# Kernel optimization log

Hardware: AMD Instinct MI355X
Metric: run time of the kernel (lower is better)

## Reference

```python
import jax, jax.numpy as jnp
import numpy as np

MAX_NUM_CENTERS = 100
CENTER_IGNORE_PX = 3
SIGMA = 2.0   # center_gt_blur
KSIZE = 21    # GaussianLayer kernel size (ReflectionPad2d(10) + Conv2d(k=21))


def _gauss_kernel():
    r = KSIZE // 2
    x = jnp.arange(-r, r + 1, dtype=jnp.float32)
    g = jnp.exp(-0.5 * (x / SIGMA) ** 2)
    g = g / g.sum()
    return jnp.outer(g, g)  # [21,21], sums to 1 (matches scipy gaussian_filter of a delta)


def _gaussian_blur(x):
    # x: [B,H,W] -> depthwise 21x21 gaussian with reflect padding (GaussianLayer)
    r = KSIZE // 2
    k = _gauss_kernel()[None, None]  # [1,1,21,21]
    xp = jnp.pad(x[:, None], ((0, 0), (0, 0), (r, r), (r, r)), mode="reflect")
    y = jax.lax.conv_general_dilated(xp, k, (1, 1), "VALID",
                                     dimension_numbers=("NCHW", "OIHW", "NCHW"))
    return y[:, 0]


def setup_inputs() -> dict:
    key = jax.random.key(0)
    k1, k2 = jax.random.split(key)
    B, H, W = 8, 768, 768
    instances = jax.random.randint(k1, (B, 1, H, W), 0, MAX_NUM_CENTERS, dtype=jnp.int32)
    centers = jax.random.uniform(k2, (B, MAX_NUM_CENTERS, 2), dtype=jnp.float32) * (H - 1) + 1.0
    return {"instances": instances, "centers": centers}


def reference(instances, centers):
    B, _, H, W = instances.shape
    inst = instances[:, 0]                                # [B,H,W]
    col = jnp.arange(W, dtype=jnp.float32)                # xym_s[0][i,j] = j
    row = jnp.arange(H, dtype=jnp.float32)[:, None]       # xym_s[1][i,j] = i

    valid = inst > 0                                      # instance_mask
    has_inst = jnp.any(valid, axis=(1, 2)).astype(jnp.float32)  # len(unique)>1 gate

    # per-pixel nearest-center gather: center = centers[b, id-1]
    idx = jnp.clip(inst - 1, 0, MAX_NUM_CENTERS - 1)
    c = centers[jnp.arange(B)[:, None, None], idx]        # [B,H,W,2]
    gt_cx = jnp.where(valid, c[..., 1], -10000.0)         # gt_center_x (swapped coords)
    gt_cy = jnp.where(valid, c[..., 0], -10000.0)

    gt_X = gt_cx - row                                    # gt_center_x - xym_s[1]
    gt_Y = gt_cy - col                                    # gt_center_y - xym_s[0]

    near = (jnp.abs(gt_X) < CENTER_IGNORE_PX) & (jnp.abs(gt_Y) < CENTER_IGNORE_PX)
    # batches with no instances skip the block -> ignore stays all-ones
    ignore = jnp.where(has_inst[:, None, None] > 0, (~near).astype(jnp.float32), 1.0)

    m = valid.astype(jnp.float32)
    R = jnp.sqrt(gt_X ** 2 + gt_Y ** 2) * m
    theta_raw = jnp.arctan2(gt_Y, gt_X)
    theta = theta_raw * has_inst[:, None, None]           # skipped (zero) when no instances
    s = jnp.sin(theta_raw) * m
    cth = jnp.cos(theta_raw) * m
    M = jnp.sqrt(s ** 2 + cth ** 2)                       # == m, kept for faithfulness
    s = jnp.where(valid, s / jnp.maximum(M, 1e-12), 0.0)
    cth = jnp.where(valid, cth / jnp.maximum(M, 1e-12), 0.0)

    # gt_center_mask: zeros if no center-neighborhood pixels, else normalized blur
    blur = _gaussian_blur(1.0 - ignore)
    all_ones = jnp.all(ignore >= 1.0, axis=(1, 2))        # gt_center_mask.all()
    bmax = jnp.max(blur, axis=(1, 2), keepdims=True)
    cmask = jnp.where(all_ones[:, None, None], 0.0, blur / jnp.maximum(bmax, 1e-12))

    top = jnp.stack([R, theta, s, cth, ignore, cmask], axis=1)       # [B,6,H,W]
    mat = jnp.concatenate([top, jnp.zeros((B, 7, H, W), top.dtype)], axis=1)[:, :, None]
    # mat: [B,13,1,H,W]; channels 6..12 are zero (no orientation input)

    # gt_centers[id] = centers[b, id-1][[1,0]] for each instance id present
    present = jnp.zeros((B, MAX_NUM_CENTERS), dtype=bool).at[
        jnp.arange(B)[:, None], inst.reshape(B, -1)].set(True)
    swapped = centers[..., ::-1]
    gt_centers = jnp.zeros_like(centers).at[:, 1:, :].set(
        jnp.where(present[:, 1:, None], swapped[:, :-1, :], 0.0))

    return mat, gt_centers
```

## Files before the change

kernel.cpp:

```cpp
#include <hip/hip_runtime.h>
#include <math.h>

#define NB 8
#define NH 768
#define NW 768
#define NHW (NH*NW)
#define NCEN 100
#define NPIX (NB*NHW)
#define RAD 10
#define KS 21

#define TS 64
#define HALO 10
#define MS (TS + 2*HALO)
#define TILES_X (NW / TS)
#define TILES_Y (NH / TS)
#define TILES_PER_B (TILES_X * TILES_Y)

#define HDR_PRESENT 0
#define HDR_HAS 32
#define HDR_NEAR 40
#define HDR_BMAX 48
#define HDR_INTS 64

__device__ __forceinline__ int refl(int i, int n) {
    i = i < 0 ? -i : i;
    return i >= n ? 2 * n - 2 - i : i;
}

__global__ void k_init(int* __restrict__ hdr) {
    int t = threadIdx.x;
    if (t < HDR_INTS) hdr[t] = 0;
}

__global__ void k_scan(const int4* __restrict__ inst4, int* __restrict__ hdr) {
    __shared__ unsigned sm[4];
    int t = threadIdx.x;
    if (t < 4) sm[t] = 0;
    __syncthreads();
    unsigned m0 = 0, m1 = 0, m2 = 0, m3 = 0;
    size_t base = (size_t)blockIdx.x * 1024 + t;
    int b = (int)((size_t)blockIdx.x * 4096 / NHW);
#pragma unroll
    for (int q = 0; q < 4; q++) {
        int4 v = inst4[base + (size_t)q * 256];
        int a[4] = {v.x, v.y, v.z, v.w};
#pragma unroll
        for (int e = 0; e < 4; e++) {
            int iv = a[e];
            if (iv > 0) {
                unsigned bit = 1u << (iv & 31);
                int w = iv >> 5;
                if (w == 0) m0 |= bit; else if (w == 1) m1 |= bit;
                else if (w == 2) m2 |= bit; else m3 |= bit;
            }
        }
    }
#pragma unroll
    for (int off = 32; off >= 1; off >>= 1) {
        m0 |= __shfl_xor(m0, off);
        m1 |= __shfl_xor(m1, off);
        m2 |= __shfl_xor(m2, off);
        m3 |= __shfl_xor(m3, off);
    }
    if ((t & 63) == 0) {
        if (m0) atomicOr(&sm[0], m0);
        if (m1) atomicOr(&sm[1], m1);
        if (m2) atomicOr(&sm[2], m2);
        if (m3) atomicOr(&sm[3], m3);
    }
    __syncthreads();
    if (t < 4 && sm[t]) atomicOr((unsigned*)&hdr[HDR_PRESENT + b * 4 + t], sm[t]);
}

__global__ void k_small(const float* __restrict__ centers, int* __restrict__ hdr,
                        float* __restrict__ gt) {
    int t = threadIdx.x;
    if (t < NB * NCEN) {
        int b = t / NCEN, k = t - b * NCEN;
        float vx = 0.f, vy = 0.f;
        if (k >= 1) {
            unsigned w = (unsigned)hdr[HDR_PRESENT + b * 4 + (k >> 5)];
            if ((w >> (k & 31)) & 1u) {
                vx = centers[(b * NCEN + (k - 1)) * 2 + 1];
                vy = centers[(b * NCEN + (k - 1)) * 2 + 0];
            }
        }
        gt[t * 2 + 0] = vx;
        gt[t * 2 + 1] = vy;
    } else if (t < NB * NCEN + NB) {
        int b = t - NB * NCEN;
        unsigned any = ((unsigned)hdr[HDR_PRESENT + b * 4] & 0xFFFFFFFEu)
                     | (unsigned)hdr[HDR_PRESENT + b * 4 + 1]
                     | (unsigned)hdr[HDR_PRESENT + b * 4 + 2]
                     | (unsigned)hdr[HDR_PRESENT + b * 4 + 3];
        hdr[HDR_HAS + b] = any ? 1 : 0;
    }
}

__global__ __launch_bounds__(256) void k_fused(const int* __restrict__ inst,
                                               const float* __restrict__ centers,
                                               int* __restrict__ hdr,
                                               float* __restrict__ out) {
    __shared__ float s_cen[2 * NCEN];
    __shared__ float s_mask[MS * MS];
    __shared__ float s_hbuf[MS * TS];
    __shared__ float s_w[KS];
    __shared__ float s_red[4];

    int t = threadIdx.x;
    int tile = blockIdx.x;
    int b = tile / TILES_PER_B;
    int tr = tile - b * TILES_PER_B;
    int ti0 = (tr / TILES_X) * TS;
    int tj0 = (tr - (tr / TILES_X) * TILES_X) * TS;

    if (t == 0) {
        float v[KS];
        float sum = 0.f;
        for (int k = 0; k < KS; k++) {
            float x = (float)(k - RAD) * 0.5f;
            v[k] = expf(-0.5f * x * x);
            sum += v[k];
        }
        for (int k = 0; k < KS; k++) s_w[k] = v[k] / sum;
    }
    for (int k = t; k < 2 * NCEN; k += 256) s_cen[k] = centers[b * 2 * NCEN + k];
    int has = hdr[HDR_HAS + b];
    __syncthreads();

    int anynear = 0;
    const int* instb = inst + (size_t)b * NHW;
    for (int e = t; e < MS * MS; e += 256) {
        int r = e / MS, c = e - r * MS;
        int gi = refl(ti0 + r - HALO, NH);
        int gj = refl(tj0 + c - HALO, NW);
        int iv = instb[gi * NW + gj];
        float mv = 0.f;
        if (has && iv > 0) {
            int idx = iv - 1;
            float cy = s_cen[2 * idx];
            float cx = s_cen[2 * idx + 1];
            float X = cx - (float)gi;
            float Y = cy - (float)gj;
            if (fabsf(X) < 3.f && fabsf(Y) < 3.f) { mv = 1.f; anynear = 1; }
        }
        s_mask[e] = mv;
    }
    if (anynear) hdr[HDR_NEAR + b] = 1;
    __syncthreads();

    for (int e = t; e < MS * TS; e += 256) {
        int r = e >> 6, c = e & 63;
        const float* mrow = &s_mask[r * MS + c];
        float acc = 0.f;
#pragma unroll
        for (int k = 0; k < KS; k++) acc += s_w[k] * mrow[k];
        s_hbuf[e] = acc;
    }
    __syncthreads();

    float wmax = 0.f;
    float* outb = out + (size_t)b * 13 * NHW;
    for (int e = t; e < TS * TS; e += 256) {
        int r = e >> 6, c = e & 63;
        float blur = 0.f;
#pragma unroll
        for (int k = 0; k < KS; k++) blur += s_w[k] * s_hbuf[(r + k) * TS + c];
        wmax = fmaxf(wmax, blur);

        int gi = ti0 + r, gj = tj0 + c;
        int p = gi * NW + gj;
        int iv = instb[p];
        bool valid = iv > 0;
        int idx = iv - 1;
        idx = idx < 0 ? 0 : idx;
        float cy = s_cen[2 * idx];
        float cx = s_cen[2 * idx + 1];
        float gcx = valid ? cx : -10000.f;
        float gcy = valid ? cy : -10000.f;
        float X = gcx - (float)gi;
        float Y = gcy - (float)gj;
        bool near = (fabsf(X) < 3.f) && (fabsf(Y) < 3.f);
        float ignore = (has != 0) ? (near ? 0.f : 1.f) : 1.f;
        float m = valid ? 1.f : 0.f;
        float R2 = X * X + Y * Y;
        float R = sqrtf(R2) * m;
        float rinv = R2 > 0.f ? rsqrtf(R2) : 0.f;
        float s = valid ? Y * rinv : 0.f;
        float cth = valid ? (R2 > 0.f ? X * rinv : 1.f) : 0.f;
        float th = atan2f(Y, X);
        float theta = (has != 0) ? th : 0.f;

        size_t base = (size_t)p;
        outb[base + 0 * (size_t)NHW] = R;
        outb[base + 1 * (size_t)NHW] = theta;
        outb[base + 2 * (size_t)NHW] = s;
        outb[base + 3 * (size_t)NHW] = cth;
        outb[base + 4 * (size_t)NHW] = ignore;
        outb[base + 5 * (size_t)NHW] = blur;
#pragma unroll
        for (int ch = 6; ch < 13; ++ch) outb[base + (size_t)ch * NHW] = 0.f;
    }

#pragma unroll
    for (int off = 32; off >= 1; off >>= 1) wmax = fmaxf(wmax, __shfl_down(wmax, off));
    if ((t & 63) == 0) s_red[t >> 6] = wmax;
    __syncthreads();
    if (t == 0) {
        float bm = fmaxf(fmaxf(s_red[0], s_red[1]), fmaxf(s_red[2], s_red[3]));
        atomicMax((unsigned*)&hdr[HDR_BMAX + b], __float_as_uint(bm));
    }
}

__global__ void k_norm(const int* __restrict__ hdr, float* __restrict__ out) {
    int g = blockIdx.x * 256 + threadIdx.x;
    int b = g / (NHW / 4);
    int p4 = g - b * (NHW / 4);
    float4* c5 = (float4*)(out + (size_t)b * 13 * NHW + 5 * (size_t)NHW);
    float4 v = c5[p4];
    float bm = __uint_as_float((unsigned)hdr[HDR_BMAX + b]);
    float sc = (hdr[HDR_NEAR + b] != 0) ? 1.f / fmaxf(bm, 1e-12f) : 0.f;
    v.x *= sc; v.y *= sc; v.z *= sc; v.w *= sc;
    c5[p4] = v;
}

extern "C" void kernel_launch(void* const* d_in, const int* in_sizes, int n_in,
                              void* d_out, int out_size, void* d_ws, size_t ws_size,
                              hipStream_t stream) {
    const int* inst = (const int*)d_in[0];
    const float* centers = (const float*)d_in[1];
    float* out = (float*)d_out;
    int* hdr = (int*)d_ws;
    float* gt = out + (size_t)NB * 13 * NHW;

    k_init<<<1, 64, 0, stream>>>(hdr);
    k_scan<<<NPIX / 4096, 256, 0, stream>>>((const int4*)inst, hdr);
    k_small<<<1, 1024, 0, stream>>>(centers, hdr, gt);
    k_fused<<<NB * TILES_PER_B, 256, 0, stream>>>(inst, centers, hdr, out);
    k_norm<<<NPIX / 1024, 256, 0, stream>>>(hdr, out);
}
```

Before: 300.9 us.

## Vectorize output stores with nontemporal float4 writes and drop init kernel

The fused kernel's output loop now has each thread handle four adjacent pixels. It reads instances as int4, does the vertical blur as a float4 accumulation, and writes all 13 channels with 128-bit nontemporal stores instead of scalar stores. The scan kernel now writes per-block presence masks without atomics. k_small reduces those masks and also zeroes the header fields, so the separate init kernel launch goes away. This is meant to cut store-instruction count and launch overhead. The risk is that nontemporal writes to channel 5 may make the later k_norm read-modify-write miss in cache.

Result: no change. 300.8 us (-0.0%).

```diff
diff --git a/kernel.cpp b/kernel.cpp
--- a/kernel.cpp
+++ b/kernel.cpp
@@ -14,23 +14,20 @@
 #define HALO 10
 #define MS (TS + 2*HALO)
 #define TILES_X (NW / TS)
-#define TILES_Y (NH / TS)
-#define TILES_PER_B (TILES_X * TILES_Y)
-
-#define HDR_PRESENT 0
+#define TILES_PER_B (TILES_X * TILES_X)
+#define SCAN_BLKS (NPIX / 4096)
+#define BLKS_PER_B (NHW / 4096)
+
 #define HDR_HAS 32
 #define HDR_NEAR 40
 #define HDR_BMAX 48
-#define HDR_INTS 64
+#define HDR_BLOCKMASK 64
+
+typedef float f4 __attribute__((ext_vector_type(4)));
 
 __device__ __forceinline__ int refl(int i, int n) {
     i = i < 0 ? -i : i;
     return i >= n ? 2 * n - 2 - i : i;
-}
-
-__global__ void k_init(int* __restrict__ hdr) {
-    int t = threadIdx.x;
-    if (t < HDR_INTS) hdr[t] = 0;
 }
 
 __global__ void k_scan(const int4* __restrict__ inst4, int* __restrict__ hdr) {
@@ -40,7 +37,6 @@
     __syncthreads();
     unsigned m0 = 0, m1 = 0, m2 = 0, m3 = 0;
     size_t base = (size_t)blockIdx.x * 1024 + t;
-    int b = (int)((size_t)blockIdx.x * 4096 / NHW);
 #pragma unroll
     for (int q = 0; q < 4; q++) {
         int4 v = inst4[base + (size_t)q * 256];
@@ -70,17 +66,27 @@
         if (m3) atomicOr(&sm[3], m3);
     }
     __syncthreads();
-    if (t < 4 && sm[t]) atomicOr((unsigned*)&hdr[HDR_PRESENT + b * 4 + t], sm[t]);
+    if (t < 4) ((unsigned*)&hdr[HDR_BLOCKMASK])[blockIdx.x * 4 + t] = sm[t];
 }
 
 __global__ void k_small(const float* __restrict__ centers, int* __restrict__ hdr,
                         float* __restrict__ gt) {
+    __shared__ unsigned s_pres[32];
     int t = threadIdx.x;
+    const unsigned* bm = (const unsigned*)&hdr[HDR_BLOCKMASK];
+    if (t < 32) {
+        int b = t >> 2, wi = t & 3;
+        unsigned acc = 0;
+        for (int k = 0; k < BLKS_PER_B; k++) acc |= bm[(b * BLKS_PER_B + k) * 4 + wi];
+        s_pres[t] = acc;
+    }
+    if (t >= 40 && t < 56) hdr[t] = 0;
+    __syncthreads();
     if (t < NB * NCEN) {
         int b = t / NCEN, k = t - b * NCEN;
         float vx = 0.f, vy = 0.f;
         if (k >= 1) {
-            unsigned w = (unsigned)hdr[HDR_PRESENT + b * 4 + (k >> 5)];
+            unsigned w = s_pres[b * 4 + (k >> 5)];
             if ((w >> (k & 31)) & 1u) {
                 vx = centers[(b * NCEN + (k - 1)) * 2 + 1];
                 vy = centers[(b * NCEN + (k - 1)) * 2 + 0];
@@ -90,10 +96,8 @@
         gt[t * 2 + 1] = vy;
     } else if (t < NB * NCEN + NB) {
         int b = t - NB * NCEN;
-        unsigned any = ((unsigned)hdr[HDR_PRESENT + b * 4] & 0xFFFFFFFEu)
-                     | (unsigned)hdr[HDR_PRESENT + b * 4 + 1]
-                     | (unsigned)hdr[HDR_PRESENT + b * 4 + 2]
-                     | (unsigned)hdr[HDR_PRESENT + b * 4 + 3];
+        unsigned any = (s_pres[b * 4] & 0xFFFFFFFEu)
+                     | s_pres[b * 4 + 1] | s_pres[b * 4 + 2] | s_pres[b * 4 + 3];
         hdr[HDR_HAS + b] = any ? 1 : 0;
     }
 }
@@ -162,45 +166,55 @@
 
     float wmax = 0.f;
     float* outb = out + (size_t)b * 13 * NHW;
-    for (int e = t; e < TS * TS; e += 256) {
-        int r = e >> 6, c = e & 63;
-        float blur = 0.f;
-#pragma unroll
-        for (int k = 0; k < KS; k++) blur += s_w[k] * s_hbuf[(r + k) * TS + c];
-        wmax = fmaxf(wmax, blur);
-
-        int gi = ti0 + r, gj = tj0 + c;
-        int p = gi * NW + gj;
-        int iv = instb[p];
-        bool valid = iv > 0;
-        int idx = iv - 1;
-        idx = idx < 0 ? 0 : idx;
-        float cy = s_cen[2 * idx];
-        float cx = s_cen[2 * idx + 1];
-        float gcx = valid ? cx : -10000.f;
-        float gcy = valid ? cy : -10000.f;
-        float X = gcx - (float)gi;
-        float Y = gcy - (float)gj;
-        bool near = (fabsf(X) < 3.f) && (fabsf(Y) < 3.f);
-        float ignore = (has != 0) ? (near ? 0.f : 1.f) : 1.f;
-        float m = valid ? 1.f : 0.f;
-        float R2 = X * X + Y * Y;
-        float R = sqrtf(R2) * m;
-        float rinv = R2 > 0.f ? rsqrtf(R2) : 0.f;
-        float s = valid ? Y * rinv : 0.f;
-        float cth = valid ? (R2 > 0.f ? X * rinv : 1.f) : 0.f;
-        float th = atan2f(Y, X);
-        float theta = (has != 0) ? th : 0.f;
-
-        size_t base = (size_t)p;
-        outb[base + 0 * (size_t)NHW] = R;
-        outb[base + 1 * (size_t)NHW] = theta;
-        outb[base + 2 * (size_t)NHW] = s;
-        outb[base + 3 * (size_t)NHW] = cth;
-        outb[base + 4 * (size_t)NHW] = ignore;
-        outb[base + 5 * (size_t)NHW] = blur;
-#pragma unroll
-        for (int ch = 6; ch < 13; ++ch) outb[base + (size_t)ch * NHW] = 0.f;
+    for (int q = t; q < TS * TS / 4; q += 256) {
+        int r = q >> 4;
+        int c0 = (q & 15) * 4;
+        f4 blur = {0.f, 0.f, 0.f, 0.f};
+#pragma unroll
+        for (int k = 0; k < KS; k++) {
+            f4 hv = *(const f4*)&s_hbuf[(r + k) * TS + c0];
+            blur += s_w[k] * hv;
+        }
+        wmax = fmaxf(wmax, fmaxf(fmaxf(blur.x, blur.y), fmaxf(blur.z, blur.w)));
+
+        int gi = ti0 + r, gj0 = tj0 + c0;
+        int p0 = gi * NW + gj0;
+        int4 ivv = *(const int4*)&instb[p0];
+        int ia[4] = {ivv.x, ivv.y, ivv.z, ivv.w};
+        f4 vR, vTh, vS, vC, vIg;
+#pragma unroll
+        for (int e = 0; e < 4; e++) {
+            int iv = ia[e];
+            bool valid = iv > 0;
+            int idx = iv - 1;
+            idx = idx < 0 ? 0 : idx;
+            float cy = s_cen[2 * idx];
+            float cx = s_cen[2 * idx + 1];
+            float gcx = valid ? cx : -10000.f;
+            float gcy = valid ? cy : -10000.f;
+            float X = gcx - (float)gi;
+            float Y = gcy - (float)(gj0 + e);
+            bool near = (fabsf(X) < 3.f) && (fabsf(Y) < 3.f);
+            vIg[e] = (has != 0) ? (near ? 0.f : 1.f) : 1.f;
+            float m = valid ? 1.f : 0.f;
+            float R2 = X * X + Y * Y;
+            vR[e] = sqrtf(R2) * m;
+            float rinv = R2 > 0.f ? rsqrtf(R2) : 0.f;
+            vS[e] = valid ? Y * rinv : 0.f;
+            vC[e] = valid ? (R2 > 0.f ? X * rinv : 1.f) : 0.f;
+            float th = atan2f(Y, X);
+            vTh[e] = (has != 0) ? th : 0.f;
+        }
+        __builtin_nontemporal_store(vR,   (f4*)&outb[(size_t)0 * NHW + p0]);
+        __builtin_nontemporal_store(vTh,  (f4*)&outb[(size_t)1 * NHW + p0]);
+        __builtin_nontemporal_store(vS,   (f4*)&outb[(size_t)2 * NHW + p0]);
+        __builtin_nontemporal_store(vC,   (f4*)&outb[(size_t)3 * NHW + p0]);
+        __builtin_nontemporal_store(vIg,  (f4*)&outb[(size_t)4 * NHW + p0]);
+        __builtin_nontemporal_store(blur, (f4*)&outb[(size_t)5 * NHW + p0]);
+        f4 z = {0.f, 0.f, 0.f, 0.f};
+#pragma unroll
+        for (int ch = 6; ch < 13; ++ch)
+            __builtin_nontemporal_store(z, (f4*)&outb[(size_t)ch * NHW + p0]);
     }
 
 #pragma unroll
@@ -208,8 +222,8 @@
     if ((t & 63) == 0) s_red[t >> 6] = wmax;
     __syncthreads();
     if (t == 0) {
-        float bm = fmaxf(fmaxf(s_red[0], s_red[1]), fmaxf(s_red[2], s_red[3]));
-        atomicMax((unsigned*)&hdr[HDR_BMAX + b], __float_as_uint(bm));
+        float bmx = fmaxf(fmaxf(s_red[0], s_red[1]), fmaxf(s_red[2], s_red[3]));
+        atomicMax((unsigned*)&hdr[HDR_BMAX + b], __float_as_uint(bmx));
     }
 }
 
@@ -217,11 +231,11 @@
     int g = blockIdx.x * 256 + threadIdx.x;
     int b = g / (NHW / 4);
     int p4 = g - b * (NHW / 4);
-    float4* c5 = (float4*)(out + (size_t)b * 13 * NHW + 5 * (size_t)NHW);
-    float4 v = c5[p4];
+    f4* c5 = (f4*)(out + (size_t)b * 13 * NHW + 5 * (size_t)NHW);
+    f4 v = c5[p4];
     float bm = __uint_as_float((unsigned)hdr[HDR_BMAX + b]);
     float sc = (hdr[HDR_NEAR + b] != 0) ? 1.f / fmaxf(bm, 1e-12f) : 0.f;
-    v.x *= sc; v.y *= sc; v.z *= sc; v.w *= sc;
+    v *= sc;
     c5[p4] = v;
 }
 
@@ -234,8 +248,7 @@
     int* hdr = (int*)d_ws;
     float* gt = out + (size_t)NB * 13 * NHW;
 
-    k_init<<<1, 64, 0, stream>>>(hdr);
-    k_scan<<<NPIX / 4096, 256, 0, stream>>>((const int4*)inst, hdr);
+    k_scan<<<SCAN_BLKS, 256, 0, stream>>>((const int4*)inst, hdr);
     k_small<<<1, 1024, 0, stream>>>(centers, hdr, gt);
     k_fused<<<NB * TILES_PER_B, 256, 0, stream>>>(inst, centers, hdr, out);
     k_norm<<<NPIX / 1024, 256, 0, stream>>>(hdr, out);
```
